# Kernel optimization log

Hardware: AMD Instinct MI355X
Metric: run time of the kernel (lower is better)

## Reference

```python
import jax, jax.numpy as jnp
import numpy as np

B, S, HID = 1, 4096, 2048
NH, NKV, HD, RD = 16, 4, 128, 64
EPS = 1e-6
SCALE = HD ** -0.5


def _rmsnorm(x, w, eps=EPS):
    x32 = x.astype(jnp.float32)
    var = jnp.mean(x32 * x32, axis=-1, keepdims=True)
    return (w * (x32 * jax.lax.rsqrt(var + eps))).astype(x.dtype)


def _rotate_half(x):
    x1, x2 = jnp.split(x, 2, axis=-1)
    return jnp.concatenate([-x2, x1], axis=-1)


def setup_inputs() -> dict:
    key = jax.random.key(0)
    ks = jax.random.split(key, 6)
    hidden_states = jax.random.normal(ks[0], (B, S, HID), dtype=jnp.float32)
    # real rotary embeddings for rotary_dim=RD
    inv_freq = 1.0 / (10000.0 ** (jnp.arange(0, RD, 2, dtype=jnp.float32) / RD))
    pos = jnp.arange(S, dtype=jnp.float32)
    freqs = pos[:, None] * inv_freq[None, :]          # [S, RD/2]
    emb = jnp.concatenate([freqs, freqs], axis=-1)     # [S, RD]
    cos = jnp.cos(emb)[None]                           # [1, S, RD]
    sin = jnp.sin(emb)[None]
    w = 0.02
    Wq = jax.random.normal(ks[1], (NH * HD, HID), dtype=jnp.float32) * w
    Wk = jax.random.normal(ks[2], (NKV * HD, HID), dtype=jnp.float32) * w
    Wv = jax.random.normal(ks[3], (NKV * HD, HID), dtype=jnp.float32) * w
    Wo = jax.random.normal(ks[4], (HID, NH * HD), dtype=jnp.float32) * w
    q_norm_w = jnp.ones((NH * HD,), dtype=jnp.float32)
    k_norm_w = jnp.ones((NKV * HD,), dtype=jnp.float32)
    return {"hidden_states": hidden_states, "cos": cos, "sin": sin,
            "Wq": Wq, "Wk": Wk, "Wv": Wv, "Wo": Wo,
            "q_norm_w": q_norm_w, "k_norm_w": k_norm_w}


def _attention(hidden_states, cos, sin, Wq, Wk, Wv, Wo, q_norm_w, k_norm_w):
    bsz, q_len, _ = hidden_states.shape
    q = hidden_states @ Wq.T                 # [B,S,NH*HD]
    k = hidden_states @ Wk.T                 # [B,S,NKV*HD]
    v = hidden_states @ Wv.T
    q = _rmsnorm(q, q_norm_w)
    k = _rmsnorm(k, k_norm_w)
    q = q.reshape(bsz, q_len, NH, HD).transpose(0, 2, 1, 3)   # b h s d
    k = k.reshape(bsz, q_len, NKV, HD).transpose(0, 2, 1, 3)
    v = v.reshape(bsz, q_len, NKV, HD).transpose(0, 2, 1, 3)
    # partial RoPE on first RD dims
    c = cos[:, None]  # [B,1,S,RD]
    s = sin[:, None]
    q_rot, q_pass = q[..., :RD], q[..., RD:]
    k_rot, k_pass = k[..., :RD], k[..., RD:]
    q = jnp.concatenate([q_rot * c + _rotate_half(q_rot) * s, q_pass], axis=-1)
    k = jnp.concatenate([k_rot * c + _rotate_half(k_rot) * s, k_pass], axis=-1)
    # GQA: repeat kv heads
    n_rep = NH // NKV
    k = jnp.repeat(k, n_rep, axis=1)
    v = jnp.repeat(v, n_rep, axis=1)
    scores = jnp.einsum('bhqd,bhkd->bhqk', q, k) * SCALE
    causal = jnp.triu(jnp.full((q_len, q_len), -jnp.inf, dtype=scores.dtype), k=1)
    scores = scores + causal
    probs = jax.nn.softmax(scores.astype(jnp.float32), axis=-1).astype(q.dtype)
    out = jnp.einsum('bhqk,bhkd->bhqd', probs, v)
    out = out.transpose(0, 2, 1, 3).reshape(bsz, q_len, NH * HD)
    return out @ Wo.T


def reference(hidden_states, cos, sin, Wq, Wk, Wv, Wo, q_norm_w, k_norm_w):
    return _attention(hidden_states, cos, sin, Wq, Wk, Wv, Wo, q_norm_w, k_norm_w)
```

## Files before the change

kernel.cpp:

```cpp
#include <hip/hip_runtime.h>

typedef unsigned short u16;
typedef unsigned int   u32;
typedef __bf16 bf16x8 __attribute__((ext_vector_type(8)));
typedef float  f32x4  __attribute__((ext_vector_type(4)));

#define S_LEN 4096
#define HIDN  2048
#define NHEAD 16
#define NKVH  4
#define HDIM  128
#define ROTD  64
#define QKVN  3072

__device__ __forceinline__ u16 f2bf(float f) {
  union { float f; u32 u; } v; v.f = f;
  u32 r = v.u + 0x7FFFu + ((v.u >> 16) & 1u);
  return (u16)(r >> 16);
}
__device__ __forceinline__ u16 f2bf_fast(float f) {
  union { __bf16 b; u16 u; } cv; cv.b = (__bf16)f; return cv.u;
}
__device__ __forceinline__ float bf2f(u16 u) {
  union { u32 u; float f; } v; v.u = ((u32)u) << 16; return v.f;
}
__device__ __forceinline__ void gl2lds16(const u16* g, u16* l) {
  __builtin_amdgcn_global_load_lds((const __attribute__((address_space(1))) void*)g,
                                   (__attribute__((address_space(3))) void*)l, 16, 0, 0);
}
__device__ __forceinline__ f32x4 mfma_bf16(bf16x8 a, bf16x8 b, f32x4 c) {
  return __builtin_amdgcn_mfma_f32_16x16x32_bf16(a, b, c, 0, 0, 0);
}
template <int N> __device__ __forceinline__ void vmwait() {
  if constexpr (N == 7)      asm volatile("s_waitcnt vmcnt(7)" ::: "memory");
  else if constexpr (N == 6) asm volatile("s_waitcnt vmcnt(6)" ::: "memory");
  else                       asm volatile("s_waitcnt vmcnt(0)" ::: "memory");
}

__global__ __launch_bounds__(256) void cvt_f32_bf16(const float* __restrict__ in,
                                                    u16* __restrict__ out) {
  size_t i = ((size_t)blockIdx.x * 256 + threadIdx.x) * 8;
  float4 a = *(const float4*)(in + i);
  float4 b = *(const float4*)(in + i + 4);
  uint4 r;
  r.x = (u32)f2bf(a.x) | ((u32)f2bf(a.y) << 16);
  r.y = (u32)f2bf(a.z) | ((u32)f2bf(a.w) << 16);
  r.z = (u32)f2bf(b.x) | ((u32)f2bf(b.y) << 16);
  r.w = (u32)f2bf(b.z) | ((u32)f2bf(b.w) << 16);
  *(uint4*)(out + i) = r;
}

template <int BN, int NB, bool BF16OUT>
__global__ __launch_bounds__(512, 2) void gemm_big(const u16* __restrict__ A,
                                                   const u16* __restrict__ Bm,
                                                   void* __restrict__ Cp,
                                                   int M, int N, int K) {
  constexpr int WNC = BN / 4;
  constexpr int NF  = WNC / 16;
  constexpr int ASZ = 256 * 128;
  constexpr int BUF = ASZ + BN * 128;
  constexpr int LOADS = 4 + NB;
  __shared__ __align__(1024) char lds[2 * BUF];

  const int tid = threadIdx.x, wave = tid >> 6, lane = tid & 63;
  const int wm = wave >> 2, wn = wave & 3;
  const int row0 = blockIdx.x * 256, col0 = blockIdx.y * BN;
  const int l8 = lane >> 3, l7 = lane & 7;
  const int T = K >> 6;

  const u16* gA[4]; const u16* gB[NB];
  u16* ldsA[4]; u16* ldsB[NB];
  #pragma unroll
  for (int i = 0; i < 4; ++i) {
    gA[i]  = A + (size_t)(row0 + wave * 32 + i * 8 + l8) * K + (l7 ^ l8) * 8;
    ldsA[i] = (u16*)(lds + wave * 4096 + i * 1024);
  }
  #pragma unroll
  for (int i = 0; i < NB; ++i) {
    gB[i]  = Bm + (size_t)(col0 + wave * (BN / 8) + i * 8 + l8) * K + (l7 ^ l8) * 8;
    ldsB[i] = (u16*)(lds + ASZ + wave * (BN * 16) + i * 1024);
  }
  auto stage = [&](int buf, int t) {
    const size_t ko = (size_t)t * 64;
    #pragma unroll
    for (int i = 0; i < 4; ++i)
      gl2lds16(gA[i] + ko, (u16*)((char*)ldsA[i] + buf * BUF));
    #pragma unroll
    for (int i = 0; i < NB; ++i)
      gl2lds16(gB[i] + ko, (u16*)((char*)ldsB[i] + buf * BUF));
  };

  const int colx0 = (((lane >> 4))     ^ l7) * 16;
  const int colx1 = ((4 + (lane >> 4)) ^ l7) * 16;
  const char* aB = lds + (wm * 128 + (lane & 15)) * 128;
  const char* bB = lds + ASZ + (wn * WNC + (lane & 15)) * 128;

  f32x4 acc[8][NF];
  #pragma unroll
  for (int i = 0; i < 8; ++i)
    #pragma unroll
    for (int j = 0; j < NF; ++j) { f32x4 z = {0.f,0.f,0.f,0.f}; acc[i][j] = z; }

  stage(0, 0);
  stage(1, 1);
  vmwait<LOADS>();
  __builtin_amdgcn_s_barrier();

  for (int t = 0; t < T; ++t) {
    const int bo = (t & 1) * BUF;
    #pragma unroll
    for (int kh = 0; kh < 2; ++kh) {
      const int cx = kh ? colx1 : colx0;
      bf16x8 bfr[NF];
      #pragma unroll
      for (int nf = 0; nf < NF; ++nf)
        bfr[nf] = *(const bf16x8*)(bB + bo + nf * 2048 + cx);
      #pragma unroll
      for (int mh = 0; mh < 2; ++mh) {
        bf16x8 af[4];
        #pragma unroll
        for (int mf = 0; mf < 4; ++mf)
          af[mf] = *(const bf16x8*)(aB + bo + mh * 8192 + mf * 2048 + cx);
        __builtin_amdgcn_s_setprio(1);
        #pragma unroll
        for (int mf = 0; mf < 4; ++mf)
          #pragma unroll
          for (int nf = 0; nf < NF; ++nf)
            acc[mh * 4 + mf][nf] = mfma_bf16(af[mf], bfr[nf], acc[mh * 4 + mf][nf]);
        __builtin_amdgcn_s_setprio(0);
      }
    }
    asm volatile("s_waitcnt lgkmcnt(0)" ::: "memory");
    __builtin_amdgcn_s_barrier();
    if (t + 2 < T) stage(t & 1, t + 2);
    if (t + 1 < T) {
      if (t + 2 < T) vmwait<LOADS>();
      else           vmwait<0>();
      __builtin_amdgcn_s_barrier();
    }
  }

  const int mwv = row0 + wm * 128, nwv = col0 + wn * WNC;
  #pragma unroll
  for (int mf8 = 0; mf8 < 8; ++mf8)
    #pragma unroll
    for (int nf = 0; nf < NF; ++nf)
      #pragma unroll
      for (int r = 0; r < 4; ++r) {
        int m = mwv + (mf8 >> 2) * 64 + (mf8 & 3) * 16 + (lane >> 4) * 4 + r;
        int n = nwv + nf * 16 + (lane & 15);
        float v = acc[mf8][nf][r];
        if (BF16OUT) ((u16*)Cp)[(size_t)m * N + n] = f2bf(v);
        else         ((float*)Cp)[(size_t)m * N + n] = v;
      }
}

__global__ __launch_bounds__(256) void norm_rope(const u16* __restrict__ qkv,
                                                 const float* __restrict__ cosb,
                                                 const float* __restrict__ sinb,
                                                 const float* __restrict__ qw,
                                                 const float* __restrict__ kw,
                                                 u16* __restrict__ Qo,
                                                 u16* __restrict__ Ko) {
  const int s = blockIdx.x, t = threadIdx.x;
  const int wave = t >> 6, lane = t & 63;
  const float SL = 0.08838834764831845f * 1.4426950408889634f;
  __shared__ float rowbuf[HIDN];
  __shared__ float red[4];
  const u16* base = qkv + (size_t)s * QKVN;

  float x[8];
  {
    uint4 v = *(const uint4*)(base + t * 8);
    u32 w4[4] = {v.x, v.y, v.z, v.w};
    #pragma unroll
    for (int j = 0; j < 4; ++j) {
      x[2*j]   = bf2f((u16)(w4[j] & 0xffffu));
      x[2*j+1] = bf2f((u16)(w4[j] >> 16));
    }
  }
  float ss = 0.f;
  #pragma unroll
  for (int j = 0; j < 8; ++j) ss += x[j] * x[j];
  #pragma unroll
  for (int m = 1; m < 64; m <<= 1) ss += __shfl_xor(ss, m);
  if (lane == 0) red[wave] = ss;
  __syncthreads();
  float rs = rsqrtf((red[0]+red[1]+red[2]+red[3]) * (1.0f / HIDN) + 1e-6f);
  #pragma unroll
  for (int j = 0; j < 8; ++j) rowbuf[t*8 + j] = x[j] * rs * qw[t*8 + j];
  __syncthreads();
  {
    int i0 = t * 8, d0 = i0 & (HDIM - 1), hh = i0 >> 7;
    float o[8];
    if (d0 < ROTD) {
      #pragma unroll
      for (int j = 0; j < 8; ++j) {
        int d = d0 + j;
        float rot = (d < 32) ? -rowbuf[i0 + j + 32] : rowbuf[i0 + j - 32];
        o[j] = rowbuf[i0 + j] * cosb[s*ROTD + d] + rot * sinb[s*ROTD + d];
      }
    } else {
      #pragma unroll
      for (int j = 0; j < 8; ++j) o[j] = rowbuf[i0 + j];
    }
    uint4 r;
    r.x = (u32)f2bf(o[0]*SL) | ((u32)f2bf(o[1]*SL) << 16);
    r.y = (u32)f2bf(o[2]*SL) | ((u32)f2bf(o[3]*SL) << 16);
    r.z = (u32)f2bf(o[4]*SL) | ((u32)f2bf(o[5]*SL) << 16);
    r.w = (u32)f2bf(o[6]*SL) | ((u32)f2bf(o[7]*SL) << 16);
    *(uint4*)(Qo + ((size_t)hh * S_LEN + s) * HDIM + d0) = r;
  }

  const u16* kbase = base + HIDN;
  float y0, y1;
  { u32 v = *(const u32*)(kbase + t * 2); y0 = bf2f((u16)(v & 0xffffu)); y1 = bf2f((u16)(v >> 16)); }
  float ss2 = y0*y0 + y1*y1;
  #pragma unroll
  for (int m = 1; m < 64; m <<= 1) ss2 += __shfl_xor(ss2, m);
  __syncthreads();
  if (lane == 0) red[wave] = ss2;
  __syncthreads();
  float rs2 = rsqrtf((red[0]+red[1]+red[2]+red[3]) * (1.0f / 512.0f) + 1e-6f);
  rowbuf[t*2]     = y0 * rs2 * kw[t*2];
  rowbuf[t*2 + 1] = y1 * rs2 * kw[t*2 + 1];
  __syncthreads();
  {
    int i0 = t * 2, d0 = i0 & (HDIM - 1), hh = i0 >> 7;
    float o0, o1;
    if (d0 < ROTD) {
      float r0 = (d0 < 32) ? -rowbuf[i0 + 32] : rowbuf[i0 - 32];
      float r1 = (d0 + 1 < 32) ? -rowbuf[i0 + 1 + 32] : rowbuf[i0 + 1 - 32];
      o0 = rowbuf[i0]     * cosb[s*ROTD + d0]     + r0 * sinb[s*ROTD + d0];
      o1 = rowbuf[i0 + 1] * cosb[s*ROTD + d0 + 1] + r1 * sinb[s*ROTD + d0 + 1];
    } else { o0 = rowbuf[i0]; o1 = rowbuf[i0 + 1]; }
    u32 r = (u32)f2bf(o0) | ((u32)f2bf(o1) << 16);
    *(u32*)(Ko + ((size_t)hh * S_LEN + s) * HDIM + d0) = r;
  }
}

__global__ __launch_bounds__(256) void vtrans(const u16* __restrict__ qkv,
                                              u16* __restrict__ Vt) {
  const int sb = blockIdx.x * 64, db = blockIdx.y * 64, kvh = blockIdx.z;
  __shared__ u16 tile[64][72];
  const int t = threadIdx.x;
  {
    int r = t >> 2, cc = (t & 3) * 16;
    const u16* src = qkv + (size_t)(sb + r) * QKVN + 2560 + kvh * HDIM + db + cc;
    *(uint4*)&tile[r][cc]     = *(const uint4*)(src);
    *(uint4*)&tile[r][cc + 8] = *(const uint4*)(src + 8);
  }
  __syncthreads();
  {
    int d = t >> 2, sc = (t & 3) * 16;
    u16 tmp[16];
    #pragma unroll
    for (int j = 0; j < 16; ++j) tmp[j] = tile[sc + j][d];
    u16* dst = Vt + ((size_t)kvh * HDIM + db + d) * S_LEN + sb + sc;
    *(uint4*)dst       = *(uint4*)&tmp[0];
    *(uint4*)(dst + 8) = *(uint4*)&tmp[8];
  }
}

__global__ __launch_bounds__(256, 2) void attn_fwd(const u16* __restrict__ Q,
                                                   const u16* __restrict__ K,
                                                   const u16* __restrict__ Vt,
                                                   u16* __restrict__ O) {
  const int n    = blockIdx.x;
  const int slot = n & 7, kq = n >> 3;
  const int kvh  = slot >> 1;
  const int h    = kvh * 4 + (slot & 1) * 2 + (kq & 1);
  const int p    = kq >> 1;
  const int tid = threadIdx.x, wave = tid >> 6, lane = tid & 63;
  const int rh   = wave & 1;
  const int kvh2 = wave >> 1;
  __shared__ u16 Ks[2][64][128];
  __shared__ u16 Vs[2][128][64];
  __shared__ u16 Ps[2][32][64];

  const u16* gKb[4]; const u16* gVb[4];
  #pragma unroll
  for (int i = 0; i < 4; ++i) {
    int cc = wave * 4 + i;
    int rk = cc * 4 + (lane >> 4);
    gKb[i] = K + ((size_t)kvh * S_LEN + rk) * HDIM + ((lane & 15) ^ (rk & 7)) * 8;
    int rv = cc * 8 + (lane >> 3);
    gVb[i] = Vt + ((size_t)kvh * HDIM + rv) * S_LEN + ((lane & 7) ^ (rv & 7)) * 8;
  }
  auto stage = [&](int buf, int kvb) {
    #pragma unroll
    for (int i = 0; i < 4; ++i) {
      int cc = wave * 4 + i;
      gl2lds16(gKb[i] + (size_t)kvb * HDIM, &Ks[buf][cc * 4][0]);
      gl2lds16(gVb[i] + kvb,                &Vs[buf][cc * 8][0]);
    }
  };

  int offv[4];
  #pragma unroll
  for (int kk = 0; kk < 4; ++kk)
    offv[kk] = (kk * 64 + (lane >> 4) * 16) ^ ((lane & 7) << 4);
  const char* ksB = (const char*)Ks + kvh2 * 8192 + (lane & 15) * 256;
  const char* vsB = (const char*)Vs + (lane & 15) * 128;
  const char* psB = (const char*)Ps + rh * 4096 + (lane & 15) * 128;
  char*       pwB = (char*)Ps + rh * 4096;
  const int   lx2 = (lane & 15) * 2;
  const int   vko = offv[kvh2];

  stage(0, 0);
  __syncthreads();
  int cur = 0;

  for (int job = 0; job < 2; ++job) {
    const int qb = job ? (63 - p) : p;
    const int ntiles = qb + 1;
    const int qg0 = qb * 64 + rh * 32 + (lane >> 4) * 4;

    bf16x8 qf[2][4];
    #pragma unroll
    for (int qm = 0; qm < 2; ++qm) {
      const u16* qptr = Q + ((size_t)h * S_LEN + qb * 64 + rh * 32 + qm * 16 + (lane & 15)) * HDIM
                        + (lane >> 4) * 8;
      #pragma unroll
      for (int kk = 0; kk < 4; ++kk) qf[qm][kk] = *(const bf16x8*)(qptr + kk * 32);
    }

    float lsum[2][4];
    #pragma unroll
    for (int qm = 0; qm < 2; ++qm)
      #pragma unroll
      for (int r = 0; r < 4; ++r) lsum[qm][r] = 0.f;
    f32x4 o[2][8];
    #pragma unroll
    for (int qm = 0; qm < 2; ++qm)
      #pragma unroll
      for (int i = 0; i < 8; ++i) { f32x4 z = {0.f,0.f,0.f,0.f}; o[qm][i] = z; }

    for (int kt = 0; kt < ntiles; ++kt) {
      if (kt + 1 < ntiles)      stage(cur ^ 1, (kt + 1) * 64);
      else if (job == 0)        stage(cur ^ 1, 0);

      const int bufo = cur << 14;
      const bool diag = (kt == ntiles - 1);

      if (!(diag && kvh2 == 1 && rh == 0)) {
        f32x4 sc[2][2];
        #pragma unroll
        for (int qm = 0; qm < 2; ++qm)
          #pragma unroll
          for (int i = 0; i < 2; ++i) { f32x4 z = {0.f,0.f,0.f,0.f}; sc[qm][i] = z; }
        __builtin_amdgcn_s_setprio(1);
        #pragma unroll
        for (int kk = 0; kk < 4; ++kk)
          #pragma unroll
          for (int nf = 0; nf < 2; ++nf) {
            bf16x8 kf = *(const bf16x8*)(ksB + bufo + nf * 4096 + offv[kk]);
            sc[0][nf] = mfma_bf16(qf[0][kk], kf, sc[0][nf]);
            sc[1][nf] = mfma_bf16(qf[1][kk], kf, sc[1][nf]);
          }
        __builtin_amdgcn_s_setprio(0);

        if (diag) {
          const int kvb = kt * 64;
          #pragma unroll
          for (int qm = 0; qm < 2; ++qm)
            #pragma unroll
            for (int nf = 0; nf < 2; ++nf) {
              int col = kvb + kvh2 * 32 + nf * 16 + (lane & 15);
              #pragma unroll
              for (int r = 0; r < 4; ++r) {
                float e = __builtin_amdgcn_exp2f(sc[qm][nf][r]);
                e = (col <= qg0 + qm * 16 + r) ? e : 0.f;
                sc[qm][nf][r] = e;
                lsum[qm][r] += e;
              }
            }
        } else {
          #pragma unroll
          for (int qm = 0; qm < 2; ++qm)
            #pragma unroll
            for (int nf = 0; nf < 2; ++nf)
              #pragma unroll
              for (int r = 0; r < 4; ++r) {
                float e = __builtin_amdgcn_exp2f(sc[qm][nf][r]);
                sc[qm][nf][r] = e;
                lsum[qm][r] += e;
              }
        }

        #pragma unroll
        for (int qm = 0; qm < 2; ++qm)
          #pragma unroll
          for (int nf = 0; nf < 2; ++nf)
            #pragma unroll
            for (int r = 0; r < 4; ++r) {
              int prow = qm * 16 + (lane >> 4) * 4 + r;
              int bcol = (kvh2 * 64 + nf * 32 + lx2) ^ ((prow & 7) << 4);
              *(u16*)(pwB + prow * 128 + bcol) = f2bf_fast(sc[qm][nf][r]);
            }

        bf16x8 pf0, pf1;
        pf0 = *(const bf16x8*)(psB + vko);
        pf1 = *(const bf16x8*)(psB + 2048 + vko);
        __builtin_amdgcn_s_setprio(1);
        #pragma unroll
        for (int nf2 = 0; nf2 < 8; ++nf2) {
          bf16x8 vf = *(const bf16x8*)(vsB + bufo + nf2 * 2048 + vko);
          o[0][nf2] = mfma_bf16(pf0, vf, o[0][nf2]);
          o[1][nf2] = mfma_bf16(pf1, vf, o[1][nf2]);
        }
        __builtin_amdgcn_s_setprio(0);
      }

      __syncthreads();
      cur ^= 1;
    }

    {
      f32x4* scr = (f32x4*)((rh == 0) ? (char*)Ks + (cur ^ 1) * 16384
                                      : (char*)Vs + (cur ^ 1) * 16384);
      float* lsc = (float*)Ps;
      if (kvh2 == 1) {
        #pragma unroll
        for (int qm = 0; qm < 2; ++qm)
          #pragma unroll
          for (int nf2 = 0; nf2 < 8; ++nf2)
            scr[(qm * 8 + nf2) * 64 + lane] = o[qm][nf2];
        #pragma unroll
        for (int qm = 0; qm < 2; ++qm)
          #pragma unroll
          for (int r = 0; r < 4; ++r)
            lsc[rh * 512 + (qm * 4 + r) * 64 + lane] = lsum[qm][r];
      }
      __syncthreads();
      if (kvh2 == 0) {
        #pragma unroll
        for (int qm = 0; qm < 2; ++qm)
          #pragma unroll
          for (int nf2 = 0; nf2 < 8; ++nf2)
            o[qm][nf2] += scr[(qm * 8 + nf2) * 64 + lane];
        #pragma unroll
        for (int qm = 0; qm < 2; ++qm)
          #pragma unroll
          for (int r = 0; r < 4; ++r)
            lsum[qm][r] += lsc[rh * 512 + (qm * 4 + r) * 64 + lane];

        #pragma unroll
        for (int qm = 0; qm < 2; ++qm)
          #pragma unroll
          for (int r = 0; r < 4; ++r) {
            float lt = lsum[qm][r];
            #pragma unroll
            for (int m = 1; m < 16; m <<= 1) lt += __shfl_xor(lt, m);
            float inv = 1.f / lt;
            int srow = qg0 + qm * 16 + r;
            #pragma unroll
            for (int nf2 = 0; nf2 < 8; ++nf2) {
              int col = h * HDIM + nf2 * 16 + (lane & 15);
              O[(size_t)srow * HIDN + col] = f2bf_fast(o[qm][nf2][r] * inv);
            }
          }
      }
      __syncthreads();
    }
  }
}

extern "C" void kernel_launch(void* const* d_in, const int* in_sizes, int n_in,
                              void* d_out, int out_size, void* d_ws, size_t ws_size,
                              hipStream_t stream) {
  (void)in_sizes; (void)n_in; (void)out_size; (void)ws_size;
  const float* h    = (const float*)d_in[0];
  const float* cosb = (const float*)d_in[1];
  const float* sinb = (const float*)d_in[2];
  const float* Wq   = (const float*)d_in[3];
  const float* Wk   = (const float*)d_in[4];
  const float* Wv   = (const float*)d_in[5];
  const float* Wo   = (const float*)d_in[6];
  const float* qw   = (const float*)d_in[7];
  const float* kw   = (const float*)d_in[8];
  float* out = (float*)d_out;

  char* ws = (char*)d_ws;
  u16* hbf  = (u16*)(ws);
  u16* Kb   = (u16*)(ws + (16u << 20));
  u16* Vtb  = (u16*)(ws + (20u << 20));
  u16* wqkv = (u16*)(ws + (24u << 20));
  u16* Qb   = (u16*)(ws + (24u << 20));
  u16* qkvb = (u16*)(ws + (40u << 20));
  u16* wob  = (u16*)(ws + (40u << 20));

  cvt_f32_bf16<<<4096, 256, 0, stream>>>(h, hbf);
  cvt_f32_bf16<<<2048, 256, 0, stream>>>(Wq, wqkv);
  cvt_f32_bf16<<<512, 256, 0, stream>>>(Wk, wqkv + 4u * 1024 * 1024);
  cvt_f32_bf16<<<512, 256, 0, stream>>>(Wv, wqkv + 5u * 1024 * 1024);

  gemm_big<192, 3, true><<<dim3(16, 16), 512, 0, stream>>>(hbf, wqkv, qkvb,
                                                           4096, 3072, 2048);

  norm_rope<<<4096, 256, 0, stream>>>(qkvb, cosb, sinb, qw, kw, Qb, Kb);
  vtrans<<<dim3(64, 2, 4), 256, 0, stream>>>(qkvb, Vtb);

  cvt_f32_bf16<<<2048, 256, 0, stream>>>(Wo, wob);

  attn_fwd<<<dim3(512), 256, 0, stream>>>(Qb, Kb, Vtb, hbf);

  gemm_big<128, 2, false><<<dim3(16, 16), 512, 0, stream>>>(hbf, wob, out,
                                                            4096, 2048, 2048);
}
```

Measured before the change: 240.7 us.

## Merge input conversions, add per-half barriers in GEMM, use fast bf16 cast

Four separate fp32-to-bf16 conversion launches are merged into one kernel that chooses its source by block index, which removes launch overhead. In the GEMM inner loop, a barrier plus LDS wait is now placed before each MFMA cluster and another barrier after it, replacing the single barrier at the end of the tile. This is meant to keep waves in lockstep so LDS reads interleave better with MFMA work, but it adds many more barriers per tile. The bf16 output store now uses the hardware cast instead of manual rounding.

```diff
diff --git a/kernel.cpp b/kernel.cpp
--- a/kernel.cpp
+++ b/kernel.cpp
@@ -35,6 +35,29 @@
   if constexpr (N == 7)      asm volatile("s_waitcnt vmcnt(7)" ::: "memory");
   else if constexpr (N == 6) asm volatile("s_waitcnt vmcnt(6)" ::: "memory");
   else                       asm volatile("s_waitcnt vmcnt(0)" ::: "memory");
+}
+
+__global__ __launch_bounds__(256) void cvt4_f32_bf16(const float* __restrict__ h,
+                                                     const float* __restrict__ Wq,
+                                                     const float* __restrict__ Wk,
+                                                     const float* __restrict__ Wv,
+                                                     u16* __restrict__ hbf,
+                                                     u16* __restrict__ wqkv) {
+  const int b = blockIdx.x;
+  const float* src; u16* dst;
+  if (b < 4096)      { src = h  + (size_t)b * 2048;           dst = hbf  + (size_t)b * 2048; }
+  else if (b < 6144) { src = Wq + (size_t)(b - 4096) * 2048;  dst = wqkv + (size_t)(b - 4096) * 2048; }
+  else if (b < 6656) { src = Wk + (size_t)(b - 6144) * 2048;  dst = wqkv + 4194304u + (size_t)(b - 6144) * 2048; }
+  else               { src = Wv + (size_t)(b - 6656) * 2048;  dst = wqkv + 5242880u + (size_t)(b - 6656) * 2048; }
+  size_t i = (size_t)threadIdx.x * 8;
+  float4 a = *(const float4*)(src + i);
+  float4 c = *(const float4*)(src + i + 4);
+  uint4 r;
+  r.x = (u32)f2bf(a.x) | ((u32)f2bf(a.y) << 16);
+  r.y = (u32)f2bf(a.z) | ((u32)f2bf(a.w) << 16);
+  r.z = (u32)f2bf(c.x) | ((u32)f2bf(c.y) << 16);
+  r.w = (u32)f2bf(c.z) | ((u32)f2bf(c.w) << 16);
+  *(uint4*)(dst + i) = r;
 }
 
 __global__ __launch_bounds__(256) void cvt_f32_bf16(const float* __restrict__ in,
@@ -121,6 +144,8 @@
         #pragma unroll
         for (int mf = 0; mf < 4; ++mf)
           af[mf] = *(const bf16x8*)(aB + bo + mh * 8192 + mf * 2048 + cx);
+        __builtin_amdgcn_s_barrier();
+        asm volatile("s_waitcnt lgkmcnt(0)" ::: "memory");
         __builtin_amdgcn_s_setprio(1);
         #pragma unroll
         for (int mf = 0; mf < 4; ++mf)
@@ -128,10 +153,9 @@
           for (int nf = 0; nf < NF; ++nf)
             acc[mh * 4 + mf][nf] = mfma_bf16(af[mf], bfr[nf], acc[mh * 4 + mf][nf]);
         __builtin_amdgcn_s_setprio(0);
+        __builtin_amdgcn_s_barrier();
       }
     }
-    asm volatile("s_waitcnt lgkmcnt(0)" ::: "memory");
-    __builtin_amdgcn_s_barrier();
     if (t + 2 < T) stage(t & 1, t + 2);
     if (t + 1 < T) {
       if (t + 2 < T) vmwait<LOADS>();
@@ -150,7 +174,7 @@
         int m = mwv + (mf8 >> 2) * 64 + (mf8 & 3) * 16 + (lane >> 4) * 4 + r;
         int n = nwv + nf * 16 + (lane & 15);
         float v = acc[mf8][nf][r];
-        if (BF16OUT) ((u16*)Cp)[(size_t)m * N + n] = f2bf(v);
+        if (BF16OUT) ((u16*)Cp)[(size_t)m * N + n] = f2bf_fast(v);
         else         ((float*)Cp)[(size_t)m * N + n] = v;
       }
 }
@@ -490,10 +514,7 @@
   u16* qkvb = (u16*)(ws + (40u << 20));
   u16* wob  = (u16*)(ws + (40u << 20));
 
-  cvt_f32_bf16<<<4096, 256, 0, stream>>>(h, hbf);
-  cvt_f32_bf16<<<2048, 256, 0, stream>>>(Wq, wqkv);
-  cvt_f32_bf16<<<512, 256, 0, stream>>>(Wk, wqkv + 4u * 1024 * 1024);
-  cvt_f32_bf16<<<512, 256, 0, stream>>>(Wv, wqkv + 5u * 1024 * 1024);
+  cvt4_f32_bf16<<<7168, 256, 0, stream>>>(h, Wq, Wk, Wv, hbf, wqkv);
 
   gemm_big<192, 3, true><<<dim3(16, 16), 512, 0, stream>>>(hbf, wqkv, qkvb,
                                                            4096, 3072, 2048);
```

Result: no change. 240.5 us (-0.1%).
